# Performance work log

Hardware: AMD Instinct MI355X
Metric: run time of the kernel (lower is better)

The kernel has to match this reference:

```python
import jax, jax.numpy as jnp
import numpy as np

B, S, D, H, P = 4, 4096, 1024, 8, 32
K = D // H  # head_dim = 128


def setup_inputs() -> dict:
    key = jax.random.key(0)
    ks = jax.random.split(key, 12)
    f = lambda k, shape, s: jax.random.normal(k, shape, dtype=jnp.float32) * s
    return {
        "x": f(ks[0], (B, S, D), 1.0),
        "W_proj": f(ks[1], (H, K, D), 0.03),
        "resonance_freqs": f(ks[2], (H, K), 0.01),
        "pol_W": f(ks[3], (H, P, K), 0.08),
        "pol_b": jnp.zeros((H, P), jnp.float32),
        "imp_W1": f(ks[4], (16, 1), 0.5),               # Linear(1, 16)
        "imp_b1": jnp.zeros((16,), jnp.float32),
        "imp_W2": f(ks[5], (1, 16), 0.25),              # Linear(16, 1)
        "imp_b2": jnp.zeros((1,), jnp.float32),
        "out_W": f(ks[6], (D, D), 0.03),                # Linear(dim, dim)
        "out_b": jnp.zeros((D,), jnp.float32),
        "ln_g": jnp.ones((D,), jnp.float32),
        "ln_b": jnp.zeros((D,), jnp.float32),
        "causal": 1,
    }


def reference(x, W_proj, resonance_freqs, pol_W, pol_b, imp_W1, imp_b1,
              imp_W2, imp_b2, out_W, out_b, ln_g, ln_b, causal):
    Bx, Sx, Dx = x.shape
    nH = W_proj.shape[0]
    # per-head projection + resonance frequency modulation -> (B, H, S, K)
    heads = jnp.einsum('bsd,hkd->bhsk', x, W_proj)
    heads = heads * jnp.cos(resonance_freqs * jnp.pi)[None, :, None, :]

    # --- GuaXiangDuiChong: learned cross-head impedance ---
    summary = heads.mean(axis=2)                                   # (B, H, K)
    pol = jnp.tanh(jnp.einsum('bhk,hpk->bhp', summary, pol_W) + pol_b[None])
    pol = pol / jnp.maximum(jnp.linalg.norm(pol, axis=-1, keepdims=True), 1e-12)
    dots = jnp.einsum('bhp,bgp->bhg', pol, pol)                    # (B, H, H)
    z = dots[..., None]                                            # (B, H, H, 1)
    hid = jax.nn.gelu(z * imp_W1[:, 0] + imp_b1, approximate=False)  # (B, H, H, 16)
    imp = jax.nn.softplus(jnp.einsum('bijc,oc->bijo', hid, imp_W2) + imp_b2)[..., 0]
    eye = jnp.eye(nH, dtype=x.dtype)
    impedance = imp * (1.0 - eye)                                  # (B, H, H)

    # --- cross-head transfer ---
    # h_i += sum_{j != i} heads_j / (1 + imp[i,j]) * 0.1, causally mean-masked.
    coef = (0.1 / (1.0 + impedance)) * (1.0 - eye)                 # zero diagonal (i == j skipped)
    transfer = jnp.einsum('bij,bjsk->bisk', coef, heads)           # (B, H, S, K)
    if causal and Sx > 1:
        # masked_fill(t>s)+mean over t of a key-independent tensor == scale by (s+1)/S
        scale = (jnp.arange(Sx, dtype=x.dtype) + 1.0) / Sx
        transfer = transfer * scale[None, None, :, None]
    out_heads = heads + transfer

    merged = out_heads.transpose(0, 2, 1, 3).reshape(Bx, Sx, Dx)   # cat heads on last dim
    y = merged @ out_W.T + out_b + x                               # dropout is identity in eval
    mu = y.mean(-1, keepdims=True)
    var = ((y - mu) ** 2).mean(-1, keepdims=True)
    normed = (y - mu) / jnp.sqrt(var + 1e-5) * ln_g + ln_b
    return normed, impedance
```

## Files before the change

kernel.cpp:

```cpp
#include <hip/hip_runtime.h>

typedef __bf16 bf16x8 __attribute__((ext_vector_type(8)));
typedef float f32x4 __attribute__((ext_vector_type(4)));
typedef unsigned short us8 __attribute__((ext_vector_type(8)));

#define PI_F 3.14159265358979323846f

__device__ __forceinline__ unsigned short f2bf(float f) {
    unsigned u = __float_as_uint(f);
    u += 0x7FFFu + ((u >> 16) & 1u);
    return (unsigned short)(u >> 16);
}
__device__ __forceinline__ float bf2f(unsigned short h) {
    return __uint_as_float(((unsigned)h) << 16);
}

__device__ __forceinline__ void async16(const void* g, void* l) {
    __builtin_amdgcn_global_load_lds(
        (const __attribute__((address_space(1))) unsigned int*)g,
        (__attribute__((address_space(3))) unsigned int*)l, 16, 0, 0);
}

__global__ __launch_bounds__(256) void prep_k(const float* __restrict__ W,
                                              const float* __restrict__ fr,
                                              const float* __restrict__ Wo,
                                              unsigned short* __restrict__ W1b,
                                              unsigned short* __restrict__ Wob) {
    int idx = blockIdx.x * 256 + threadIdx.x;
    if (idx < (1 << 20)) {
        int n = idx >> 10, d = idx & 1023;
        int k = n >> 3, h = n & 7;
        float c = cosf(fr[h * 128 + k] * PI_F);
        W1b[idx] = f2bf(W[((h * 128 + k) << 10) + d] * c);
    } else {
        int i2 = idx - (1 << 20);
        int n = i2 >> 10, dp = i2 & 1023;
        int k = dp >> 3, h = dp & 7;
        Wob[i2] = f2bf(Wo[(n << 10) + h * 128 + k]);
    }
}

__global__ __launch_bounds__(256) void xbar_cast(const float* __restrict__ x,
                                                 unsigned short* __restrict__ xb,
                                                 float* __restrict__ part) {
    int bid = blockIdx.x;
    int b = bid >> 8;
    int s0 = (bid & 255) * 16;
    int t = threadIdx.x;
    float a0 = 0.f, a1 = 0.f, a2 = 0.f, a3 = 0.f;
    for (int i = 0; i < 16; ++i) {
        long row = (long)b * 4096 + s0 + i;
        float4 v = ((const float4*)x)[row * 256 + t];
        a0 += v.x; a1 += v.y; a2 += v.z; a3 += v.w;
        ushort4 u;
        u.x = f2bf(v.x); u.y = f2bf(v.y); u.z = f2bf(v.z); u.w = f2bf(v.w);
        ((ushort4*)xb)[row * 256 + t] = u;
    }
    float4 p; p.x = a0; p.y = a1; p.z = a2; p.w = a3;
    ((float4*)part)[bid * 256 + t] = p;
}

__global__ __launch_bounds__(256) void xbar_r(const float* __restrict__ part,
                                              float* __restrict__ xbar) {
    __shared__ float sl[256];
    int blk = blockIdx.x;
    int b = blk >> 3, dgrp = blk & 7;
    int t = threadIdx.x;
    int col = dgrp * 128 + (t & 127);
    int ih = t >> 7;
    float s = 0.f;
    for (int i = 0; i < 128; ++i) {
        int cb = b * 256 + ih * 128 + i;
        s += part[cb * 1024 + col];
    }
    sl[t] = s;
    __syncthreads();
    if (t < 128) xbar[b * 1024 + col] = sl[t] + sl[t + 128];
}

__global__ __launch_bounds__(256) void summary_k(const float* __restrict__ xbar,
                                                 const float* __restrict__ W,
                                                 const float* __restrict__ fr,
                                                 float* __restrict__ summary) {
    int wave = (blockIdx.x * 256 + threadIdx.x) >> 6;
    int lane = threadIdx.x & 63;
    int b = wave >> 10, hk = wave & 1023;
    int h = hk >> 7, k = hk & 127;
    const float* wrow = &W[(h * 128 + k) << 10];
    const float* xrow = &xbar[b << 10];
    float s = 0.f;
    for (int d = lane; d < 1024; d += 64) s += xrow[d] * wrow[d];
    for (int off = 32; off; off >>= 1) s += __shfl_down(s, off);
    if (lane == 0) {
        float c = cosf(fr[h * 128 + k] * PI_F);
        summary[wave] = s * c * (1.0f / 4096.0f);
    }
}

__global__ __launch_bounds__(256) void imp_k(const float* __restrict__ summary,
                                             const float* __restrict__ pol_W,
                                             const float* __restrict__ pol_b,
                                             const float* __restrict__ imp_W1,
                                             const float* __restrict__ imp_b1,
                                             const float* __restrict__ imp_W2,
                                             const float* __restrict__ imp_b2,
                                             float* __restrict__ coef_out,
                                             float* __restrict__ imp_out) {
    __shared__ float pol[4][8][32];
    __shared__ float rn[32];
    int t = threadIdx.x;
    for (int o = t; o < 1024; o += 256) {
        int b = o >> 8, h = (o >> 5) & 7, p = o & 31;
        const float* srow = &summary[(b * 8 + h) * 128];
        const float* wrow = &pol_W[(h * 32 + p) * 128];
        float acc = pol_b[h * 32 + p];
        for (int k = 0; k < 128; ++k) acc += srow[k] * wrow[k];
        pol[b][h][p] = tanhf(acc);
    }
    __syncthreads();
    if (t < 32) {
        int b = t >> 3, h = t & 7;
        float ss = 0.f;
        for (int p = 0; p < 32; ++p) { float v = pol[b][h][p]; ss += v * v; }
        rn[t] = 1.0f / fmaxf(sqrtf(ss), 1e-12f);
    }
    __syncthreads();
    {
        int b = t >> 6, i = (t >> 3) & 7, j = t & 7;
        float d = 0.f;
        for (int p = 0; p < 32; ++p) d += pol[b][i][p] * pol[b][j][p];
        d *= rn[b * 8 + i] * rn[b * 8 + j];
        float s = imp_b2[0];
        for (int c = 0; c < 16; ++c) {
            float z = d * imp_W1[c] + imp_b1[c];
            float gl = 0.5f * z * (1.0f + erff(z * 0.70710678118654752f));
            s += gl * imp_W2[c];
        }
        float sp = fmaxf(s, 0.0f) + log1pf(expf(-fabsf(s)));
        float impv = (i == j) ? 0.0f : sp;
        imp_out[t] = impv;
        coef_out[t] = (i == j) ? 0.0f : 0.1f / (1.0f + impv);
    }
}

#define VMCNT(n) asm volatile("s_waitcnt vmcnt(" #n ")" ::: "memory")
#define SBAR() __builtin_amdgcn_s_barrier()

__device__ __forceinline__ void swz256(int n, long& rowBase, long& colBase) {
    int xcd = n & 7, s = n >> 3;
    rowBase = (long)(xcd * 8 + (s & 7)) * 256;
    colBase = (long)(s >> 3) * 256;
}

#define STG(sPtr, dPtr, koff, slot)                                          \
    async16((sPtr) + (koff), (dPtr) + (slot) * 16384);                       \
    async16((sPtr) + (koff) + 262144, (dPtr) + (slot) * 16384 + 8192);

#define PH(p, DO_ST, KOFF, VM)                                               \
    {                                                                        \
        if (DO_ST) {                                                         \
            STG(sA, stDstA, (KOFF), ((p) + 2) & 3)                           \
            STG(sB, stDstB, (KOFF), ((p) + 2) & 3)                           \
        }                                                                    \
        VM;                                                                  \
        SBAR();                                                              \
        const char* pA = rdA + ((p) & 3) * 16384;                            \
        const char* pB = rdB + ((p) & 3) * 16384;                            \
        bf16x8 af[4], bv[4];                                                 \
        _Pragma("unroll") for (int i_ = 0; i_ < 4; ++i_)                     \
            af[i_] = *(const bf16x8*)(pA + i_ * 1024);                       \
        _Pragma("unroll") for (int i_ = 0; i_ < 4; ++i_)                     \
            bv[i_] = *(const bf16x8*)(pB + i_ * 1024);                       \
        __builtin_amdgcn_s_setprio(1);                                       \
        _Pragma("unroll") for (int mi = 0; mi < 4; ++mi)                     \
            _Pragma("unroll") for (int ni = 0; ni < 4; ++ni)                 \
                acc[mi][ni] = __builtin_amdgcn_mfma_f32_16x16x32_bf16(       \
                    af[mi], bv[ni], acc[mi][ni], 0, 0, 0);                   \
        __builtin_amdgcn_s_setprio(0);                                       \
        _Pragma("unroll") for (int i_ = 0; i_ < 4; ++i_)                     \
            af[i_] = *(const bf16x8*)(pA + (4 + i_) * 1024);                 \
        __builtin_amdgcn_s_setprio(1);                                       \
        _Pragma("unroll") for (int mi = 0; mi < 4; ++mi)                     \
            _Pragma("unroll") for (int ni = 0; ni < 4; ++ni)                 \
                acc[4 + mi][ni] = __builtin_amdgcn_mfma_f32_16x16x32_bf16(   \
                    af[mi], bv[ni], acc[4 + mi][ni], 0, 0, 0);               \
        __builtin_amdgcn_s_setprio(0);                                       \
    }

__device__ __forceinline__ void gemm8_core(const char* gAB, const char* gBB,
                                           char* smem, const int t,
                                           f32x4 acc[8][4]) {
    const int l = t & 63, wid = t >> 6;
    const int wm = wid >> 2, wn = wid & 3;
    const long stOff = (long)((wid << 4) + (t & 15)) * 2048 + ((t >> 4) & 3) * 16;
    const char* sA = gAB + stOff;
    const char* sB = gBB + stOff;
    char* As = smem;
    char* Bs = smem + 65536;
    char* stDstA = As + wid * 1024;
    char* stDstB = Bs + wid * 1024;
    const char* rdA = As + wm * 8192 + l * 16;
    const char* rdB = Bs + wn * 4096 + l * 16;

    STG(sA, stDstA, 0, 0)
    STG(sB, stDstB, 0, 0)
    STG(sA, stDstA, 64, 1)
    STG(sB, stDstB, 64, 1)

    int kb = 128;
    for (int grp = 0; grp < 7; ++grp) {
        PH(0, true, kb, VMCNT(8))
        PH(1, true, kb + 64, VMCNT(8))
        PH(2, true, kb + 128, VMCNT(8))
        PH(3, true, kb + 192, VMCNT(8))
        kb += 256;
    }
    PH(0, true, 1920, VMCNT(8))
    PH(1, true, 1984, VMCNT(8))
    PH(2, false, 0, VMCNT(4))
    PH(3, false, 0, VMCNT(0))
}

__global__ __launch_bounds__(512, 2) void gemm1_mix(
    const unsigned short* __restrict__ A, const unsigned short* __restrict__ B,
    const float* __restrict__ coef, const int* __restrict__ causal,
    unsigned short* __restrict__ C) {
    __shared__ char smem[131072];
    __shared__ float cfs[64];
    const int t = threadIdx.x;
    long rowBase, colBase;
    swz256(blockIdx.x, rowBase, colBase);
    const int b = (int)(rowBase >> 12);
    if (t < 64) cfs[t] = coef[b * 64 + t];
    const int causalv = causal[0];

    f32x4 acc[8][4] = {};
    gemm8_core((const char*)A + rowBase * 2048, (const char*)B + colBase * 2048,
               smem, t, acc);
    __syncthreads();

    const int l = t & 63, wid = t >> 6;
    const int wm = wid >> 2, wn = wid & 3;
    const int q = l >> 4, c16 = l & 15;
    float* slab = (float*)smem;
#pragma unroll
    for (int p = 0; p < 8; ++p) {
        if (wm == (p >> 2)) {
            const int m0 = (p & 3) * 2;
#pragma unroll
            for (int m2 = 0; m2 < 2; ++m2)
#pragma unroll
                for (int ni = 0; ni < 4; ++ni)
#pragma unroll
                    for (int r = 0; r < 4; ++r)
                        slab[(m2 * 16 + q * 4 + r) * 264 + wn * 64 + ni * 16 + c16] =
                            acc[m0 + m2][ni][r];
        }
        __syncthreads();
#pragma unroll
        for (int gg = 0; gg < 2; ++gg) {
            const int g = t + gg * 512;
            const int row32 = g >> 5, kg = g & 31;
            const float* src = slab + row32 * 264 + kg * 8;
            float v[8];
#pragma unroll
            for (int j = 0; j < 8; ++j) v[j] = src[j];
            const long row = rowBase + p * 32 + row32;
            const float scale =
                causalv ? (float)((row & 4095) + 1) * (1.0f / 4096.0f) : 1.0f;
            us8 o;
#pragma unroll
            for (int i = 0; i < 8; ++i) {
                float ts = 0.f;
#pragma unroll
                for (int j = 0; j < 8; ++j) ts += cfs[i * 8 + j] * v[j];
                o[i] = f2bf(v[i] + scale * ts);
            }
            *(us8*)(C + row * 1024 + colBase + kg * 8) = o;
        }
        __syncthreads();
    }
}

__global__ __launch_bounds__(512, 2) void gemm_bt(const unsigned short* __restrict__ A,
                                                  const unsigned short* __restrict__ B,
                                                  unsigned short* __restrict__ C) {
    __shared__ char smem[131072];
    const int t = threadIdx.x;
    long rowBase, colBase;
    swz256(blockIdx.x, rowBase, colBase);

    f32x4 acc[8][4] = {};
    gemm8_core((const char*)A + rowBase * 2048, (const char*)B + colBase * 2048,
               smem, t, acc);

    const int l = t & 63, wid = t >> 6;
    const int wm = wid >> 2, wn = wid & 3;
    const int q = l >> 4, c16 = l & 15;
#pragma unroll
    for (int mi = 0; mi < 8; ++mi)
#pragma unroll
        for (int ni = 0; ni < 4; ++ni) {
            const long col = colBase + wn * 64 + ni * 16 + c16;
            const long row0 = rowBase + wm * 128 + mi * 16 + q * 4;
#pragma unroll
            for (int r = 0; r < 4; ++r)
                C[(row0 + r) * 1024 + col] = f2bf(acc[mi][ni][r]);
        }
}

__global__ __launch_bounds__(256) void ln_k(const unsigned short* __restrict__ ypre,
                                            const float* __restrict__ x,
                                            const float* __restrict__ outb,
                                            const float* __restrict__ gam,
                                            const float* __restrict__ bet,
                                            float* __restrict__ out) {
    int row = blockIdx.x;
    int t = threadIdx.x;
    long base = (long)row * 1024 + t * 4;
    ushort4 yp = *(const ushort4*)(ypre + base);
    float4 xv = *(const float4*)(x + base);
    float4 bv = *(const float4*)(outb + t * 4);
    float y0 = bf2f(yp.x) + xv.x + bv.x;
    float y1 = bf2f(yp.y) + xv.y + bv.y;
    float y2 = bf2f(yp.z) + xv.z + bv.z;
    float y3 = bf2f(yp.w) + xv.w + bv.w;
    float s = y0 + y1 + y2 + y3;
    float ss = y0 * y0 + y1 * y1 + y2 * y2 + y3 * y3;
    for (int off = 32; off; off >>= 1) {
        s += __shfl_down(s, off);
        ss += __shfl_down(ss, off);
    }
    __shared__ float red[8];
    int wv = t >> 6, ln = t & 63;
    if (ln == 0) { red[wv] = s; red[4 + wv] = ss; }
    __syncthreads();
    float S1 = red[0] + red[1] + red[2] + red[3];
    float S2 = red[4] + red[5] + red[6] + red[7];
    float mu = S1 * (1.0f / 1024.0f);
    float var = S2 * (1.0f / 1024.0f) - mu * mu;
    float rs = 1.0f / sqrtf(var + 1e-5f);
    float4 gv = *(const float4*)(gam + t * 4);
    float4 bb = *(const float4*)(bet + t * 4);
    float4 o;
    o.x = (y0 - mu) * rs * gv.x + bb.x;
    o.y = (y1 - mu) * rs * gv.y + bb.y;
    o.z = (y2 - mu) * rs * gv.z + bb.z;
    o.w = (y3 - mu) * rs * gv.w + bb.w;
    *(float4*)(out + base) = o;
}

extern "C" void kernel_launch(void* const* d_in, const int* in_sizes, int n_in,
                              void* d_out, int out_size, void* d_ws, size_t ws_size,
                              hipStream_t stream) {
    const float* x       = (const float*)d_in[0];
    const float* W_proj  = (const float*)d_in[1];
    const float* freqs   = (const float*)d_in[2];
    const float* pol_W   = (const float*)d_in[3];
    const float* pol_b   = (const float*)d_in[4];
    const float* imp_W1  = (const float*)d_in[5];
    const float* imp_b1  = (const float*)d_in[6];
    const float* imp_W2  = (const float*)d_in[7];
    const float* imp_b2  = (const float*)d_in[8];
    const float* out_W   = (const float*)d_in[9];
    const float* out_b   = (const float*)d_in[10];
    const float* ln_g    = (const float*)d_in[11];
    const float* ln_b    = (const float*)d_in[12];
    const int*   causal  = (const int*)d_in[13];
    float* out = (float*)d_out;

    char* ws = (char*)d_ws;
    unsigned short* xb      = (unsigned short*)(ws + 0);
    unsigned short* merged  = (unsigned short*)(ws + 33554432);
    unsigned short* w1b     = (unsigned short*)(ws + 67108864);
    unsigned short* wob     = (unsigned short*)(ws + 69206016);
    float* xbar             = (float*)(ws + 71303168);
    float* summary          = (float*)(ws + 71319552);
    float* coef             = (float*)(ws + 71335936);
    float* part             = (float*)merged;
    unsigned short* ypre    = xb;

    prep_k<<<8192, 256, 0, stream>>>(W_proj, freqs, out_W, w1b, wob);
    xbar_cast<<<1024, 256, 0, stream>>>(x, xb, part);
    xbar_r<<<32, 256, 0, stream>>>(part, xbar);
    summary_k<<<1024, 256, 0, stream>>>(xbar, W_proj, freqs, summary);
    imp_k<<<1, 256, 0, stream>>>(summary, pol_W, pol_b, imp_W1, imp_b1,
                                 imp_W2, imp_b2, coef, out + 16777216);
    gemm1_mix<<<256, 512, 0, stream>>>(xb, w1b, coef, causal, merged);
    gemm_bt<<<256, 512, 0, stream>>>(merged, wob, ypre);
    ln_k<<<16384, 256, 0, stream>>>(ypre, x, out_b, ln_g, ln_b, out);
}
```

Measured before the change: 295.8 us.

## Shrink GEMM tiles from 256x256 to 128x128 with 4-wave blocks

Both bf16 GEMMs move from 256x256 output tiles on 512-thread blocks to 128x128 tiles on 256-thread blocks. Grid size grows from 256 to 1024 blocks and per-block LDS drops from 128KB to 64KB. The cross-head mixing epilogue in gemm1_mix now works on 16-row slabs. The goal is better occupancy and load balance across the 256 CUs, at the cost of lower arithmetic intensity and more global and L2 traffic per FLOP.

```diff
diff --git a/kernel.cpp b/kernel.cpp
--- a/kernel.cpp
+++ b/kernel.cpp
@@ -146,26 +146,26 @@
 #define VMCNT(n) asm volatile("s_waitcnt vmcnt(" #n ")" ::: "memory")
 #define SBAR() __builtin_amdgcn_s_barrier()
 
-__device__ __forceinline__ void swz256(int n, long& rowBase, long& colBase) {
+__device__ __forceinline__ void swizzle_blk(int n, long& rowBase, long& colBase) {
     int xcd = n & 7, s = n >> 3;
-    rowBase = (long)(xcd * 8 + (s & 7)) * 256;
-    colBase = (long)(s >> 3) * 256;
-}
-
-#define STG(sPtr, dPtr, koff, slot)                                          \
-    async16((sPtr) + (koff), (dPtr) + (slot) * 16384);                       \
-    async16((sPtr) + (koff) + 262144, (dPtr) + (slot) * 16384 + 8192);
+    rowBase = (long)(xcd * 16 + (s & 15)) * 128;
+    colBase = (long)(s >> 4) * 128;
+}
+
+#define STG2(sPtr, dPtr, koff, slot)                                         \
+    async16((sPtr) + (koff), (dPtr) + (slot) * 8192);                        \
+    async16((sPtr) + (koff) + 131072, (dPtr) + (slot) * 8192 + 4096);
 
 #define PH(p, DO_ST, KOFF, VM)                                               \
     {                                                                        \
         if (DO_ST) {                                                         \
-            STG(sA, stDstA, (KOFF), ((p) + 2) & 3)                           \
-            STG(sB, stDstB, (KOFF), ((p) + 2) & 3)                           \
+            STG2(sA, stDstA, (KOFF), ((p) + 2) & 3)                          \
+            STG2(sB, stDstB, (KOFF), ((p) + 2) & 3)                          \
         }                                                                    \
         VM;                                                                  \
         SBAR();                                                              \
-        const char* pA = rdA + ((p) & 3) * 16384;                            \
-        const char* pB = rdB + ((p) & 3) * 16384;                            \
+        const char* pA = rdA + ((p) & 3) * 8192;                             \
+        const char* pB = rdB + ((p) & 3) * 8192;                             \
         bf16x8 af[4], bv[4];                                                 \
         _Pragma("unroll") for (int i_ = 0; i_ < 4; ++i_)                     \
             af[i_] = *(const bf16x8*)(pA + i_ * 1024);                       \
@@ -177,35 +177,27 @@
                 acc[mi][ni] = __builtin_amdgcn_mfma_f32_16x16x32_bf16(       \
                     af[mi], bv[ni], acc[mi][ni], 0, 0, 0);                   \
         __builtin_amdgcn_s_setprio(0);                                       \
-        _Pragma("unroll") for (int i_ = 0; i_ < 4; ++i_)                     \
-            af[i_] = *(const bf16x8*)(pA + (4 + i_) * 1024);                 \
-        __builtin_amdgcn_s_setprio(1);                                       \
-        _Pragma("unroll") for (int mi = 0; mi < 4; ++mi)                     \
-            _Pragma("unroll") for (int ni = 0; ni < 4; ++ni)                 \
-                acc[4 + mi][ni] = __builtin_amdgcn_mfma_f32_16x16x32_bf16(   \
-                    af[mi], bv[ni], acc[4 + mi][ni], 0, 0, 0);               \
-        __builtin_amdgcn_s_setprio(0);                                       \
-    }
-
-__device__ __forceinline__ void gemm8_core(const char* gAB, const char* gBB,
+    }
+
+__device__ __forceinline__ void gemm4_core(const char* gAB, const char* gBB,
                                            char* smem, const int t,
-                                           f32x4 acc[8][4]) {
+                                           f32x4 acc[4][4]) {
     const int l = t & 63, wid = t >> 6;
-    const int wm = wid >> 2, wn = wid & 3;
+    const int wm = wid >> 1, wn = wid & 1;
     const long stOff = (long)((wid << 4) + (t & 15)) * 2048 + ((t >> 4) & 3) * 16;
     const char* sA = gAB + stOff;
     const char* sB = gBB + stOff;
     char* As = smem;
-    char* Bs = smem + 65536;
+    char* Bs = smem + 32768;
     char* stDstA = As + wid * 1024;
     char* stDstB = Bs + wid * 1024;
-    const char* rdA = As + wm * 8192 + l * 16;
-    const char* rdB = Bs + wn * 4096 + l * 16;
-
-    STG(sA, stDstA, 0, 0)
-    STG(sB, stDstB, 0, 0)
-    STG(sA, stDstA, 64, 1)
-    STG(sB, stDstB, 64, 1)
+    const char* rdA = As + wm * 4096 + (l >> 4) * 256 + (l & 15) * 16;
+    const char* rdB = Bs + wn * 4096 + (l >> 4) * 256 + (l & 15) * 16;
+
+    STG2(sA, stDstA, 0, 0)
+    STG2(sB, stDstB, 0, 0)
+    STG2(sA, stDstA, 64, 1)
+    STG2(sB, stDstB, 64, 1)
 
     int kb = 128;
     for (int grp = 0; grp < 7; ++grp) {
@@ -221,92 +213,84 @@
     PH(3, false, 0, VMCNT(0))
 }
 
-__global__ __launch_bounds__(512, 2) void gemm1_mix(
+__global__ __launch_bounds__(256, 2) void gemm1_mix(
     const unsigned short* __restrict__ A, const unsigned short* __restrict__ B,
     const float* __restrict__ coef, const int* __restrict__ causal,
     unsigned short* __restrict__ C) {
-    __shared__ char smem[131072];
+    __shared__ char smem[65536];
     __shared__ float cfs[64];
     const int t = threadIdx.x;
     long rowBase, colBase;
-    swz256(blockIdx.x, rowBase, colBase);
+    swizzle_blk(blockIdx.x, rowBase, colBase);
     const int b = (int)(rowBase >> 12);
     if (t < 64) cfs[t] = coef[b * 64 + t];
     const int causalv = causal[0];
 
-    f32x4 acc[8][4] = {};
-    gemm8_core((const char*)A + rowBase * 2048, (const char*)B + colBase * 2048,
+    f32x4 acc[4][4] = {};
+    gemm4_core((const char*)A + rowBase * 2048, (const char*)B + colBase * 2048,
                smem, t, acc);
-    __syncthreads();
 
     const int l = t & 63, wid = t >> 6;
-    const int wm = wid >> 2, wn = wid & 3;
+    const int wm = wid >> 1, wn = wid & 1;
     const int q = l >> 4, c16 = l & 15;
-    float* slab = (float*)smem;
+    float* mixt = (float*)smem;
+    const int r16 = t >> 4, kg = t & 15;
 #pragma unroll
     for (int p = 0; p < 8; ++p) {
         if (wm == (p >> 2)) {
-            const int m0 = (p & 3) * 2;
-#pragma unroll
-            for (int m2 = 0; m2 < 2; ++m2)
-#pragma unroll
-                for (int ni = 0; ni < 4; ++ni)
-#pragma unroll
-                    for (int r = 0; r < 4; ++r)
-                        slab[(m2 * 16 + q * 4 + r) * 264 + wn * 64 + ni * 16 + c16] =
-                            acc[m0 + m2][ni][r];
+            int mi = p & 3;
+#pragma unroll
+            for (int ni = 0; ni < 4; ++ni)
+#pragma unroll
+                for (int r = 0; r < 4; ++r)
+                    mixt[(q * 4 + r) * 132 + wn * 64 + ni * 16 + c16] = acc[mi][ni][r];
         }
         __syncthreads();
-#pragma unroll
-        for (int gg = 0; gg < 2; ++gg) {
-            const int g = t + gg * 512;
-            const int row32 = g >> 5, kg = g & 31;
-            const float* src = slab + row32 * 264 + kg * 8;
-            float v[8];
-#pragma unroll
-            for (int j = 0; j < 8; ++j) v[j] = src[j];
-            const long row = rowBase + p * 32 + row32;
-            const float scale =
-                causalv ? (float)((row & 4095) + 1) * (1.0f / 4096.0f) : 1.0f;
-            us8 o;
-#pragma unroll
-            for (int i = 0; i < 8; ++i) {
-                float ts = 0.f;
-#pragma unroll
-                for (int j = 0; j < 8; ++j) ts += cfs[i * 8 + j] * v[j];
-                o[i] = f2bf(v[i] + scale * ts);
-            }
-            *(us8*)(C + row * 1024 + colBase + kg * 8) = o;
+        const float* src = mixt + r16 * 132 + kg * 8;
+        float v[8];
+#pragma unroll
+        for (int j = 0; j < 8; ++j) v[j] = src[j];
+        long row = rowBase + p * 16 + r16;
+        float scale = causalv ? (float)((row & 4095) + 1) * (1.0f / 4096.0f) : 1.0f;
+        us8 o;
+#pragma unroll
+        for (int i = 0; i < 8; ++i) {
+            float ts = 0.f;
+#pragma unroll
+            for (int j = 0; j < 8; ++j) ts += cfs[i * 8 + j] * v[j];
+            o[i] = f2bf(v[i] + scale * ts);
         }
+        *(us8*)(C + row * 1024 + colBase + kg * 8) = o;
         __syncthreads();
     }
 }
 
-__global__ __launch_bounds__(512, 2) void gemm_bt(const unsigned short* __restrict__ A,
+__global__ __launch_bounds__(256, 2) void gemm_bt(const unsigned short* __restrict__ A,
                                                   const unsigned short* __restrict__ B,
                                                   unsigned short* __restrict__ C) {
-    __shared__ char smem[131072];
+    __shared__ char smem[65536];
     const int t = threadIdx.x;
     long rowBase, colBase;
-    swz256(blockIdx.x, rowBase, colBase);
-
-    f32x4 acc[8][4] = {};
-    gemm8_core((const char*)A + rowBase * 2048, (const char*)B + colBase * 2048,
+    swizzle_blk(blockIdx.x, rowBase, colBase);
+
+    f32x4 acc[4][4] = {};
+    gemm4_core((const char*)A + rowBase * 2048, (const char*)B + colBase * 2048,
                smem, t, acc);
 
     const int l = t & 63, wid = t >> 6;
-    const int wm = wid >> 2, wn = wid & 3;
+    const int wm = wid >> 1, wn = wid & 1;
     const int q = l >> 4, c16 = l & 15;
 #pragma unroll
-    for (int mi = 0; mi < 8; ++mi)
+    for (int mi = 0; mi < 4; ++mi) {
 #pragma unroll
         for (int ni = 0; ni < 4; ++ni) {
-            const long col = colBase + wn * 64 + ni * 16 + c16;
-            const long row0 = rowBase + wm * 128 + mi * 16 + q * 4;
+            long col = colBase + wn * 64 + ni * 16 + c16;
+            long row0 = rowBase + wm * 64 + mi * 16 + q * 4;
 #pragma unroll
             for (int r = 0; r < 4; ++r)
                 C[(row0 + r) * 1024 + col] = f2bf(acc[mi][ni][r]);
         }
+    }
 }
 
 __global__ __launch_bounds__(256) void ln_k(const unsigned short* __restrict__ ypre,
@@ -386,7 +370,7 @@
     summary_k<<<1024, 256, 0, stream>>>(xbar, W_proj, freqs, summary);
     imp_k<<<1, 256, 0, stream>>>(summary, pol_W, pol_b, imp_W1, imp_b1,
                                  imp_W2, imp_b2, coef, out + 16777216);
-    gemm1_mix<<<256, 512, 0, stream>>>(xb, w1b, coef, causal, merged);
-    gemm_bt<<<256, 512, 0, stream>>>(merged, wob, ypre);
+    gemm1_mix<<<1024, 256, 0, stream>>>(xb, w1b, coef, causal, merged);
+    gemm_bt<<<1024, 256, 0, stream>>>(merged, wob, ypre);
     ln_k<<<16384, 256, 0, stream>>>(ypre, x, out_b, ln_g, ln_b, out);
 }
```

Result: slower. 338.7 us (+14.5%).
